# Kernel tuning notes

Hardware: AMD Instinct MI355X
Metric: run time of the kernel (lower is better)

Reference implementation:

```python
import jax, jax.numpy as jnp
import numpy as np

B = 256          # games in flight
BS = 19          # board side
N2 = BS * BS     # 361 points
M = N2 * 10      # history_factor = 10 -> max moves = 3610


def setup_inputs() -> dict:
    key = jax.random.key(0)
    k = jax.random.split(key, 8)
    legal_mask = jax.random.bernoulli(k[0], 0.5, (B, BS, BS))
    # captures are sparse: few stones captured per candidate move
    capture_stone_mask = jax.random.bernoulli(k[1], 0.02, (B, N2, N2))
    current_player = jax.random.randint(k[2], (B,), 0, 2, dtype=jnp.int32)
    zpos = jax.random.randint(k[3], (N2, 3), 0, 2**31 - 1, dtype=jnp.int32)
    current_hash = jax.random.randint(k[4], (B,), 0, 2**31 - 1, dtype=jnp.int32)
    hash_history = jax.random.randint(k[5], (B, M), 0, 2**31 - 1, dtype=jnp.int32)
    move_count = jax.random.randint(k[6], (B,), 0, M, dtype=jnp.int32)
    logits = jax.random.normal(k[7], (B, BS, BS), dtype=jnp.float32)
    return dict(legal_mask=legal_mask, capture_stone_mask=capture_stone_mask,
                current_player=current_player, zpos=zpos,
                current_hash=current_hash, hash_history=hash_history,
                move_count=move_count, logits=logits)


def _super_ko_filter(legal_mask, capture_stone_mask, current_player, zpos,
                     current_hash, hash_history, move_count):
    Bb, H, W = legal_mask.shape
    n2 = H * W
    legal_flat = legal_mask.reshape(Bb, n2)                      # (B, N2)
    player = current_player.astype(jnp.int32)                    # (B,)
    zposT = zpos.T                                               # (3, N2)

    # 1) delta for placing the stone: empty-key XOR player-key
    place_old = zposT[0][None, :]                                # (1, N2)
    place_new = zposT[player + 1]                                # (B, N2) gather per-batch
    place_delta = jnp.bitwise_xor(place_old, place_new)          # (B, N2)

    # 2) delta for removing a captured opponent stone at each point
    z_opp = zposT[2 - player]                                    # opp+1 = 2-player, (B, N2)
    D = jnp.bitwise_xor(z_opp, zposT[0][None, :])                # (B, N2)

    # per candidate move, XOR the deltas of all stones it would capture
    sel = jnp.where(capture_stone_mask, D[:, None, :], jnp.int32(0))  # (B, N2, N2)
    cap_delta = jax.lax.reduce(sel, jnp.int32(0), jax.lax.bitwise_xor, (2,))  # (B, N2)

    # 3) post-move hash per candidate
    new_hash = current_hash[:, None] ^ place_delta ^ cap_delta   # (B, N2)

    # 4) reject if post-move hash appears in the (valid prefix of) history
    hist_mask = jnp.arange(hash_history.shape[1])[None, :] < move_count[:, None]  # (B, M)
    eq = (new_hash[:, :, None] == hash_history[:, None, :]) & hist_mask[:, None, :]
    is_repeat = jnp.any(eq, axis=2) & legal_flat                 # (B, N2)

    return legal_mask & ~is_repeat.reshape(Bb, H, W)


def reference(legal_mask, capture_stone_mask, current_player, zpos,
              current_hash, hash_history, move_count, logits):
    final_mask = _super_ko_filter(legal_mask, capture_stone_mask, current_player,
                                  zpos, current_hash, hash_history, move_count)
    # downstream use of the filtered mask: mask policy logits
    return jnp.where(final_mask, logits, jnp.float32(-1e9))
```

## Files before the change

kernel.cpp:

```cpp
#include <hip/hip_runtime.h>
#include <stdint.h>


#define GO_B     256
#define GO_N2    361
#define GO_M     3610
#define GO_SLABB (GO_N2 * GO_N2 * 4)
#define NSPLIT   16
#define ATHR     256
#define BTHR     512
#define TBL      1024
#define DEPTH    8

__global__ __launch_bounds__(ATHR, 4)
void scan_kernel(const int* __restrict__ cap,
                 const int* __restrict__ player,
                 const int* __restrict__ zpos,
                 uint32_t*  __restrict__ partial)
{
    __shared__ uint32_t Dl[GO_N2];
    __shared__ uint32_t capx[GO_N2];

    const int b   = blockIdx.x >> 4;
    const int q   = blockIdx.x & 15;
    const int tid = threadIdx.x;
    const int p   = player[b];

    for (int i = tid; i < GO_N2; i += ATHR) {
        uint32_t z0 = (uint32_t)zpos[i * 3 + 0];
        uint32_t zo = (uint32_t)zpos[i * 3 + 2 - p];
        Dl[i]   = zo ^ z0;
        capx[i] = 0u;
    }
    __syncthreads();

    uintptr_t p0   = (uintptr_t)cap + (size_t)b * GO_SLABB;
    uintptr_t a0   = p0 & ~(uintptr_t)15;
    const uint32_t lead   = (uint32_t)(p0 - a0);
    const uint32_t nchunk = (lead + GO_SLABB + 15u) >> 4;
    const uint32_t nq     = (nchunk + NSPLIT - 1) / NSPLIT;
    const uint32_t c0     = (uint32_t)q * nq;
    const uint32_t c1     = (c0 + nq < nchunk) ? (c0 + nq) : nchunk;
    const uint4* __restrict__ src = (const uint4*)a0;

    uint4 w[DEPTH];
    #pragma unroll
    for (int k = 0; k < DEPTH; ++k) {
        uint32_t c = c0 + (uint32_t)tid + (uint32_t)k * ATHR;
        uint4 z; z.x = 0u; z.y = 0u; z.z = 0u; z.w = 0u;
        w[k] = (c < c1) ? src[c] : z;
    }
    #pragma unroll
    for (int k = 0; k < DEPTH; ++k) {
        uint4 ww = w[k];
        if ((ww.x | ww.y | ww.z | ww.w) == 0u) continue;
        uint32_t base = (c0 + (uint32_t)tid + (uint32_t)k * ATHR) * 16u - lead;
        uint32_t dw[4] = { ww.x, ww.y, ww.z, ww.w };
        #pragma unroll
        for (int d = 0; d < 4; ++d) {
            if (dw[d] != 0u) {
                uint32_t f = base + (uint32_t)(d * 4);
                if (f < (uint32_t)GO_SLABB) {
                    uint32_t e = f >> 2;
                    uint32_t i = e / 361u;
                    uint32_t j = e - i * 361u;
                    atomicXor(&capx[i], Dl[j]);
                }
            }
        }
    }
    __syncthreads();

    uint32_t* __restrict__ dst = partial + ((size_t)b * NSPLIT + q) * GO_N2;
    for (int i = tid; i < GO_N2; i += ATHR) dst[i] = capx[i];
}

__global__ __launch_bounds__(BTHR)
void finalize_kernel(const int*      __restrict__ legal,
                     const int*      __restrict__ player,
                     const int*      __restrict__ zpos,
                     const int*      __restrict__ chash,
                     const int*      __restrict__ hist,
                     const int*      __restrict__ mcount,
                     const float*    __restrict__ logits,
                     const uint32_t* __restrict__ partial,
                     float*          __restrict__ out)
{
    __shared__ uint32_t thash[TBL];
    __shared__ int      tidx[TBL];
    __shared__ uint8_t  rep[GO_N2];
    __shared__ uint8_t  leg[GO_N2];

    const int b   = blockIdx.x;
    const int tid = threadIdx.x;
    const int p   = player[b];
    const uint32_t ch = (uint32_t)chash[b];

    for (int s = tid; s < TBL; s += BTHR) tidx[s] = -1;
    for (int i = tid; i < GO_N2; i += BTHR) {
        rep[i] = 0u;
        leg[i] = legal[(size_t)b * GO_N2 + i] != 0;
    }
    __syncthreads();

    const uint32_t* __restrict__ pp = partial + (size_t)b * NSPLIT * GO_N2;
    for (int i = tid; i < GO_N2; i += BTHR) {
        uint32_t z0 = (uint32_t)zpos[i * 3 + 0];
        uint32_t zp = (uint32_t)zpos[i * 3 + 1 + p];
        uint32_t cx = 0u;
        #pragma unroll
        for (int qq = 0; qq < NSPLIT; ++qq) cx ^= pp[i + qq * GO_N2];
        uint32_t nh = ch ^ (z0 ^ zp) ^ cx;
        if (leg[i]) {
            uint32_t s = nh & (TBL - 1);
            while (true) {
                int prev = atomicCAS(&tidx[s], -1, i);
                if (prev == -1) { thash[s] = nh; break; }
                s = (s + 1) & (TBL - 1);
            }
        }
    }
    __syncthreads();

    const int mc = mcount[b];
    for (int m = tid; m < mc; m += BTHR) {
        uint32_t h = (uint32_t)hist[(size_t)b * GO_M + m];
        uint32_t s = h & (TBL - 1);
        while (tidx[s] != -1) {
            if (thash[s] == h) rep[tidx[s]] = 1u;
            s = (s + 1) & (TBL - 1);
        }
    }
    __syncthreads();

    for (int i = tid; i < GO_N2; i += BTHR) {
        bool keep = leg[i] && !rep[i];
        out[(size_t)b * GO_N2 + i] =
            keep ? logits[(size_t)b * GO_N2 + i] : -1.0e9f;
    }
}

extern "C" void kernel_launch(void* const* d_in, const int* in_sizes, int n_in,
                              void* d_out, int out_size, void* d_ws, size_t ws_size,
                              hipStream_t stream) {
    const int*   legal  = (const int*)d_in[0];
    const int*   cap    = (const int*)d_in[1];
    const int*   player = (const int*)d_in[2];
    const int*   zpos   = (const int*)d_in[3];
    const int*   chash  = (const int*)d_in[4];
    const int*   hist   = (const int*)d_in[5];
    const int*   mcount = (const int*)d_in[6];
    const float* logits = (const float*)d_in[7];
    float*       outp   = (float*)d_out;
    uint32_t*    part   = (uint32_t*)d_ws;

    scan_kernel<<<GO_B * NSPLIT, ATHR, 0, stream>>>(cap, player, zpos, part);
    finalize_kernel<<<GO_B, BTHR, 0, stream>>>(legal, player, zpos, chash,
                                               hist, mcount, logits, part, outp);
}
```

Baseline: 220.4 us.

## Replace shared-memory atomic XOR scan with per-row wavefront shuffle reductions

The capture scan now gives each wavefront whole rows of the capture matrix, two rows at a time, and keeps the D deltas in registers. Each row is XOR-reduced with cross-lane shuffles and written straight out, so the shared-memory atomics, per-element divisions and the 16-way partial buffer are gone. The finalize kernel then reads a single XOR value per point instead of combining 16 partials. In exchange, the loads become scalar 4-byte loads instead of 16-byte vector loads, and there are fewer blocks (1024 instead of 4096), which may lower memory-level parallelism on this bandwidth-bound read of about 133 MB.

```diff
diff --git a/kernel.cpp b/kernel.cpp
--- a/kernel.cpp
+++ b/kernel.cpp
@@ -2,77 +2,71 @@
 #include <stdint.h>
 
 
-#define GO_B     256
-#define GO_N2    361
-#define GO_M     3610
-#define GO_SLABB (GO_N2 * GO_N2 * 4)
-#define NSPLIT   16
-#define ATHR     256
-#define BTHR     512
-#define TBL      1024
-#define DEPTH    8
+#define GO_B   256
+#define GO_N2  361
+#define GO_M   3610
+#define TBL    1024
+#define BTHR   512
 
-__global__ __launch_bounds__(ATHR, 4)
+__global__ __launch_bounds__(256)
 void scan_kernel(const int* __restrict__ cap,
                  const int* __restrict__ player,
                  const int* __restrict__ zpos,
-                 uint32_t*  __restrict__ partial)
+                 uint32_t*  __restrict__ capx_out)
 {
-    __shared__ uint32_t Dl[GO_N2];
-    __shared__ uint32_t capx[GO_N2];
+    const int b    = blockIdx.x >> 2;
+    const int g    = blockIdx.x & 3;
+    const int wid  = g * 4 + (threadIdx.x >> 6);
+    const int lane = threadIdx.x & 63;
+    const int p    = player[b];
 
-    const int b   = blockIdx.x >> 4;
-    const int q   = blockIdx.x & 15;
-    const int tid = threadIdx.x;
-    const int p   = player[b];
+    uint32_t D[6];
+    #pragma unroll
+    for (int s = 0; s < 6; ++s) {
+        int j = lane + 64 * s;
+        D[s] = (j < GO_N2)
+             ? ((uint32_t)zpos[j * 3 + 0] ^ (uint32_t)zpos[j * 3 + 2 - p])
+             : 0u;
+    }
 
-    for (int i = tid; i < GO_N2; i += ATHR) {
-        uint32_t z0 = (uint32_t)zpos[i * 3 + 0];
-        uint32_t zo = (uint32_t)zpos[i * 3 + 2 - p];
-        Dl[i]   = zo ^ z0;
-        capx[i] = 0u;
-    }
-    __syncthreads();
+    const int* __restrict__ base_b = cap + (size_t)b * GO_N2 * GO_N2;
 
-    uintptr_t p0   = (uintptr_t)cap + (size_t)b * GO_SLABB;
-    uintptr_t a0   = p0 & ~(uintptr_t)15;
-    const uint32_t lead   = (uint32_t)(p0 - a0);
-    const uint32_t nchunk = (lead + GO_SLABB + 15u) >> 4;
-    const uint32_t nq     = (nchunk + NSPLIT - 1) / NSPLIT;
-    const uint32_t c0     = (uint32_t)q * nq;
-    const uint32_t c1     = (c0 + nq < nchunk) ? (c0 + nq) : nchunk;
-    const uint4* __restrict__ src = (const uint4*)a0;
+    for (int i = wid; i < GO_N2; i += 32) {
+        const int  iB   = i + 16;
+        const bool hasB = (iB < GO_N2);
+        const int* __restrict__ rowA = base_b + (size_t)i  * GO_N2;
+        const int* __restrict__ rowB = base_b + (size_t)iB * GO_N2;
 
-    uint4 w[DEPTH];
-    #pragma unroll
-    for (int k = 0; k < DEPTH; ++k) {
-        uint32_t c = c0 + (uint32_t)tid + (uint32_t)k * ATHR;
-        uint4 z; z.x = 0u; z.y = 0u; z.z = 0u; z.w = 0u;
-        w[k] = (c < c1) ? src[c] : z;
-    }
-    #pragma unroll
-    for (int k = 0; k < DEPTH; ++k) {
-        uint4 ww = w[k];
-        if ((ww.x | ww.y | ww.z | ww.w) == 0u) continue;
-        uint32_t base = (c0 + (uint32_t)tid + (uint32_t)k * ATHR) * 16u - lead;
-        uint32_t dw[4] = { ww.x, ww.y, ww.z, ww.w };
+        uint32_t a0, a1, a2, a3, a4, a5;
+        uint32_t b0, b1, b2, b3, b4, b5;
+        a0 = (uint32_t)rowA[lane];
+        a1 = (uint32_t)rowA[lane + 64];
+        a2 = (uint32_t)rowA[lane + 128];
+        a3 = (uint32_t)rowA[lane + 192];
+        a4 = (uint32_t)rowA[lane + 256];
+        a5 = (lane + 320 < GO_N2) ? (uint32_t)rowA[lane + 320] : 0u;
+        b0 = hasB ? (uint32_t)rowB[lane]       : 0u;
+        b1 = hasB ? (uint32_t)rowB[lane + 64]  : 0u;
+        b2 = hasB ? (uint32_t)rowB[lane + 128] : 0u;
+        b3 = hasB ? (uint32_t)rowB[lane + 192] : 0u;
+        b4 = hasB ? (uint32_t)rowB[lane + 256] : 0u;
+        b5 = (hasB && lane + 320 < GO_N2) ? (uint32_t)rowB[lane + 320] : 0u;
+
+        uint32_t accA = (a0 ? D[0] : 0u) ^ (a1 ? D[1] : 0u) ^ (a2 ? D[2] : 0u)
+                      ^ (a3 ? D[3] : 0u) ^ (a4 ? D[4] : 0u) ^ (a5 ? D[5] : 0u);
+        uint32_t accB = (b0 ? D[0] : 0u) ^ (b1 ? D[1] : 0u) ^ (b2 ? D[2] : 0u)
+                      ^ (b3 ? D[3] : 0u) ^ (b4 ? D[4] : 0u) ^ (b5 ? D[5] : 0u);
+
         #pragma unroll
-        for (int d = 0; d < 4; ++d) {
-            if (dw[d] != 0u) {
-                uint32_t f = base + (uint32_t)(d * 4);
-                if (f < (uint32_t)GO_SLABB) {
-                    uint32_t e = f >> 2;
-                    uint32_t i = e / 361u;
-                    uint32_t j = e - i * 361u;
-                    atomicXor(&capx[i], Dl[j]);
-                }
-            }
+        for (int off = 32; off >= 1; off >>= 1) {
+            accA ^= __shfl_xor(accA, off, 64);
+            accB ^= __shfl_xor(accB, off, 64);
+        }
+        if (lane == 0) {
+            capx_out[(size_t)b * GO_N2 + i] = accA;
+            if (hasB) capx_out[(size_t)b * GO_N2 + iB] = accB;
         }
     }
-    __syncthreads();
-
-    uint32_t* __restrict__ dst = partial + ((size_t)b * NSPLIT + q) * GO_N2;
-    for (int i = tid; i < GO_N2; i += ATHR) dst[i] = capx[i];
 }
 
 __global__ __launch_bounds__(BTHR)
@@ -83,7 +77,7 @@
                      const int*      __restrict__ hist,
                      const int*      __restrict__ mcount,
                      const float*    __restrict__ logits,
-                     const uint32_t* __restrict__ partial,
+                     const uint32_t* __restrict__ capx,
                      float*          __restrict__ out)
 {
     __shared__ uint32_t thash[TBL];
@@ -103,14 +97,10 @@
     }
     __syncthreads();
 
-    const uint32_t* __restrict__ pp = partial + (size_t)b * NSPLIT * GO_N2;
     for (int i = tid; i < GO_N2; i += BTHR) {
         uint32_t z0 = (uint32_t)zpos[i * 3 + 0];
         uint32_t zp = (uint32_t)zpos[i * 3 + 1 + p];
-        uint32_t cx = 0u;
-        #pragma unroll
-        for (int qq = 0; qq < NSPLIT; ++qq) cx ^= pp[i + qq * GO_N2];
-        uint32_t nh = ch ^ (z0 ^ zp) ^ cx;
+        uint32_t nh = ch ^ (z0 ^ zp) ^ capx[(size_t)b * GO_N2 + i];
         if (leg[i]) {
             uint32_t s = nh & (TBL - 1);
             while (true) {
@@ -152,9 +142,9 @@
     const int*   mcount = (const int*)d_in[6];
     const float* logits = (const float*)d_in[7];
     float*       outp   = (float*)d_out;
-    uint32_t*    part   = (uint32_t*)d_ws;
+    uint32_t*    capx   = (uint32_t*)d_ws;
 
-    scan_kernel<<<GO_B * NSPLIT, ATHR, 0, stream>>>(cap, player, zpos, part);
+    scan_kernel<<<GO_B * 4, 256, 0, stream>>>(cap, player, zpos, capx);
     finalize_kernel<<<GO_B, BTHR, 0, stream>>>(legal, player, zpos, chash,
-                                               hist, mcount, logits, part, outp);
+                                               hist, mcount, logits, capx, outp);
 }
```

After: 237.9 us. 7.9% more time.
